# Optimization experiments

Hardware: AMD Instinct MI355X
Metric: run time of the kernel (lower is better)

Reference implementation:

```python
import jax, jax.numpy as jnp
import numpy as np

M, N = 4096, 4096  # placement density grid size (even, as the rfft-based kernel assumes)


def _expk(L):
    # precompute_expk(L): [cos(pi*k/(2L)), sin(pi*k/(2L))] stacked -> [L, 2]
    a = np.pi * np.arange(L) / (2.0 * L)
    return np.stack([np.cos(a), np.sin(a)], axis=-1).astype(np.float32)


def setup_inputs() -> dict:
    key = jax.random.key(0)
    x = jax.random.normal(key, (M, N), dtype=jnp.float32)
    return {
        "x": x,
        "expkM": jnp.asarray(_expk(M)),
        "expkN": jnp.asarray(_expk(N)),
    }


def _idct1d(x, expk):
    # Unnormalized IDCT (DCT-III with DC weight 1) along the last axis:
    #   y_u = sum_k x_k * cos(pi*k*(2u+1)/(2L))
    # Makhoul FFT trick: c_k = x_k * exp(i*pi*k/(2L)); v = L*ifft(c);
    #   y[2m] = Re(v[m]),  y[2m+1] = Re(v[L-1-m])
    L = x.shape[-1]
    ek = expk[:, 0] + 1j * expk[:, 1]            # exp(i*pi*k/(2L)), [L]
    v = (jnp.fft.ifft(x * ek, axis=-1) * L).real  # [..., L]
    half = L // 2
    even = v[..., :half]                          # y[0], y[2], ...
    odd = v[..., ::-1][..., :half]                # y[1], y[3], ... (= v[L-1], v[L-2], ...)
    return jnp.stack([even, odd], axis=-1).reshape(x.shape)


def reference(x, expkM, expkN):
    # out[u,v] = sum_{p,q} x[p,q] cos(pi*p*(2u+1)/(2M)) cos(pi*q*(2v+1)/(2N))
    t = _idct1d(x, expkN)                               # transform along N (last dim)
    out = _idct1d(t.swapaxes(-1, -2), expkM)            # transform along M
    return out.swapaxes(-1, -2)
```

## Files before the change

kernel.cpp:

```cpp
#include <hip/hip_runtime.h>
#include <stdint.h>

typedef __bf16 bf16x8_t __attribute__((ext_vector_type(8)));
typedef float f32x4_t __attribute__((ext_vector_type(4)));

__device__ __forceinline__ uint32_t f32_to_bf16_bits(float f) {
    union { float f; uint32_t u; } v; v.f = f;
    return (v.u + 0x7FFFu + ((v.u >> 16) & 1u)) >> 16;
}

__device__ __forceinline__ float bf16_bits_to_f32(uint32_t b) {
    union { uint32_t u; float f; } v; v.u = b << 16;
    return v.f;
}

__global__ void prep_kernel(const float* __restrict__ X,
                            unsigned short* __restrict__ Ae,
                            unsigned short* __restrict__ Ao,
                            unsigned short* __restrict__ Xe,
                            unsigned short* __restrict__ Xo) {
    if (blockIdx.x < 4096) {
        const int idx = blockIdx.x * 256 + threadIdx.x;
        const int sel = idx >> 19;
        const int e   = idx & ((1 << 19) - 1);
        const int n   = e >> 8;
        const int c0  = (e & 255) << 3;
        const uint32_t tn = (uint32_t)(2 * n + 1);
        unsigned short* dst = sel ? Ao : Ae;
        uint32_t packed[4];
#pragma unroll
        for (int jj = 0; jj < 4; ++jj) {
            uint32_t cA = (uint32_t)(c0 + 2 * jj);
            uint32_t cB = cA + 1;
            uint32_t r0 = ((2u * cA + (uint32_t)sel) * tn) & 16383u;
            uint32_t r1 = ((2u * cB + (uint32_t)sel) * tn) & 16383u;
            float v0 = __cosf((float)r0 * 3.8349519697141e-4f);
            float v1 = __cosf((float)r1 * 3.8349519697141e-4f);
            packed[jj] = f32_to_bf16_bits(v0) | (f32_to_bf16_bits(v1) << 16);
        }
        *(uint4*)(dst + (size_t)n * 2048 + c0) = make_uint4(packed[0], packed[1], packed[2], packed[3]);
    } else {
        const int idx = (blockIdx.x - 4096) * 256 + threadIdx.x;
        const int q   = idx >> 9;
        const int p0  = (idx & 511) << 3;
        const float4* src = (const float4*)(X + (size_t)q * 4096 + p0);
        float4 a = src[0];
        float4 b = src[1];
        uint2 ev, od;
        ev.x = f32_to_bf16_bits(a.x) | (f32_to_bf16_bits(a.z) << 16);
        ev.y = f32_to_bf16_bits(b.x) | (f32_to_bf16_bits(b.z) << 16);
        od.x = f32_to_bf16_bits(a.y) | (f32_to_bf16_bits(a.w) << 16);
        od.y = f32_to_bf16_bits(b.y) | (f32_to_bf16_bits(b.w) << 16);
        *(uint2*)(Xe + (size_t)q * 2048 + (p0 >> 1)) = ev;
        *(uint2*)(Xo + (size_t)q * 2048 + (p0 >> 1)) = od;
    }
}

#define GLL(gp, lp) __builtin_amdgcn_global_load_lds( \
        (const __attribute__((address_space(1))) uint32_t*)(gp), \
        (__attribute__((address_space(3))) uint32_t*)(lp), 16, 0, 0)

__global__ __launch_bounds__(512, 2)
void gemm256_kernel(const unsigned short* __restrict__ Ae,
                    const unsigned short* __restrict__ Ao,
                    const unsigned short* __restrict__ Be,
                    const unsigned short* __restrict__ Bo,
                    unsigned short* __restrict__ Ce,
                    unsigned short* __restrict__ Co) {
    constexpr int KD = 2048;
    __shared__ __attribute__((aligned(16))) unsigned short smem[2 * 32768];

    const int tid  = threadIdx.x;
    const int wave = tid >> 6;
    const int lane = tid & 63;
    const int wm   = wave >> 2;
    const int wn   = wave & 3;

    const int tile_m = blockIdx.y << 8;
    const int tile_c = blockIdx.x << 8;
    const int par    = blockIdx.z;

    const unsigned short* gA = (par ? Ao : Ae) + (size_t)tile_m * KD;
    const unsigned short* gB = (par ? Bo : Be) + (size_t)tile_c * KD;
    unsigned short*       gC = par ? Co : Ce;

    f32x4_t acc[8][4];
#pragma unroll
    for (int i = 0; i < 8; ++i)
#pragma unroll
        for (int j = 0; j < 4; ++j)
            acc[i][j] = (f32x4_t){0.f, 0.f, 0.f, 0.f};

    int src_off[4], lds_off[4];
#pragma unroll
    for (int k = 0; k < 4; ++k) {
        const int c   = tid + (k << 9);
        const int row = c >> 3;
        const int g   = (c & 7) ^ (row & 7);
        src_off[k] = row * KD + (g << 3);
        lds_off[k] = c << 3;
    }

    const int frow = lane & 15;
    const int sw   = frow & 7;
    const int gq   = lane >> 4;
    const int aRowB = (wm * 128 + frow) * 64;
    const int bRowB = (wn * 64  + frow) * 64;

#define STAGE_TILE(buf, kadv) do {                                            \
    _Pragma("unroll")                                                         \
    for (int k_ = 0; k_ < 4; ++k_)                                            \
        GLL(gA + (kadv) + src_off[k_], (buf) + lds_off[k_]);                  \
    _Pragma("unroll")                                                         \
    for (int k_ = 0; k_ < 4; ++k_)                                            \
        GLL(gB + (kadv) + src_off[k_], (buf) + 16384 + lds_off[k_]);          \
} while (0)

#define COMPUTE_TILE(buf) do {                                                \
    _Pragma("unroll")                                                         \
    for (int kh_ = 0; kh_ < 2; ++kh_) {                                       \
        const int so_ = (((kh_ << 2) + gq) ^ sw) << 3;                        \
        bf16x8_t af_[8], bf_[4];                                              \
        _Pragma("unroll")                                                     \
        for (int i_ = 0; i_ < 8; ++i_) af_[i_] = *(const bf16x8_t*)((buf) + aRowB + i_ * 1024 + so_); \
        _Pragma("unroll")                                                     \
        for (int j_ = 0; j_ < 4; ++j_) bf_[j_] = *(const bf16x8_t*)((buf) + 16384 + bRowB + j_ * 1024 + so_); \
        __builtin_amdgcn_s_setprio(1);                                        \
        _Pragma("unroll")                                                     \
        for (int i_ = 0; i_ < 8; ++i_)                                        \
            _Pragma("unroll")                                                 \
            for (int j_ = 0; j_ < 4; ++j_)                                    \
                acc[i_][j_] = __builtin_amdgcn_mfma_f32_16x16x32_bf16(af_[i_], bf_[j_], acc[i_][j_], 0, 0, 0); \
        __builtin_amdgcn_s_setprio(0);                                        \
    }                                                                         \
} while (0)

#define TILE_SYNC() do {                                                      \
    asm volatile("s_waitcnt vmcnt(0)" ::: "memory");                          \
    __builtin_amdgcn_s_barrier();                                             \
    asm volatile("" ::: "memory");                                            \
} while (0)

    STAGE_TILE(smem, 0);
    TILE_SYNC();

    int co = 0;
#pragma unroll 1
    for (int t = 0; t < 31; ++t) {
        STAGE_TILE(smem + (co ^ 32768), (size_t)(t + 1) << 6);
        COMPUTE_TILE(smem + co);
        TILE_SYNC();
        co ^= 32768;
    }
    COMPUTE_TILE(smem + co);

#undef STAGE_TILE
#undef COMPUTE_TILE
#undef TILE_SYNC

    const int orow = tile_m + wm * 128 + ((lane >> 4) << 2);
    const int ocol = tile_c + wn * 64 + (lane & 15);
#pragma unroll
    for (int i = 0; i < 8; ++i)
#pragma unroll
        for (int j = 0; j < 4; ++j)
#pragma unroll
            for (int r = 0; r < 4; ++r) {
                const int m = orow + i * 16 + r;
                const int w = ocol + j * 16;
                gC[(size_t)m * 4096 + w] = (unsigned short)f32_to_bf16_bits(acc[i][j][r]);
            }
}

__global__ void bfly1_kernel(const unsigned short* __restrict__ Ce,
                             const unsigned short* __restrict__ Co,
                             unsigned short* __restrict__ Te,
                             unsigned short* __restrict__ To) {
    const int m  = blockIdx.x;
    const int c0 = threadIdx.x << 4;
    const uint4 e0 = *(const uint4*)(Ce + (size_t)m * 4096 + c0);
    const uint4 e1 = *(const uint4*)(Ce + (size_t)m * 4096 + c0 + 8);
    const uint4 o0 = *(const uint4*)(Co + (size_t)m * 4096 + c0);
    const uint4 o1 = *(const uint4*)(Co + (size_t)m * 4096 + c0 + 8);
    const uint32_t eu[8] = {e0.x, e0.y, e0.z, e0.w, e1.x, e1.y, e1.z, e1.w};
    const uint32_t ou[8] = {o0.x, o0.y, o0.z, o0.w, o1.x, o1.y, o1.z, o1.w};
    uint32_t se[4], so_[4], de[4], do_[4];
#pragma unroll
    for (int u = 0; u < 4; ++u) {
        float eA = bf16_bits_to_f32(eu[2*u] & 0xFFFF),  oA = bf16_bits_to_f32(ou[2*u] & 0xFFFF);
        float eB = bf16_bits_to_f32(eu[2*u] >> 16),     oB = bf16_bits_to_f32(ou[2*u] >> 16);
        float eC = bf16_bits_to_f32(eu[2*u+1] & 0xFFFF),oC = bf16_bits_to_f32(ou[2*u+1] & 0xFFFF);
        float eD = bf16_bits_to_f32(eu[2*u+1] >> 16),   oD = bf16_bits_to_f32(ou[2*u+1] >> 16);
        se[u]  = f32_to_bf16_bits(eA + oA) | (f32_to_bf16_bits(eC + oC) << 16);
        so_[u] = f32_to_bf16_bits(eB + oB) | (f32_to_bf16_bits(eD + oD) << 16);
        de[u]  = f32_to_bf16_bits(eA - oA) | (f32_to_bf16_bits(eC - oC) << 16);
        do_[u] = f32_to_bf16_bits(eB - oB) | (f32_to_bf16_bits(eD - oD) << 16);
    }
    const size_t rs = (size_t)m * 2048 + (c0 >> 1);
    const size_t rd = (size_t)(4095 - m) * 2048 + (c0 >> 1);
    *(uint4*)(Te + rs) = make_uint4(se[0], se[1], se[2], se[3]);
    *(uint4*)(To + rs) = make_uint4(so_[0], so_[1], so_[2], so_[3]);
    *(uint4*)(Te + rd) = make_uint4(de[0], de[1], de[2], de[3]);
    *(uint4*)(To + rd) = make_uint4(do_[0], do_[1], do_[2], do_[3]);
}

__global__ void bfly2_kernel(const unsigned short* __restrict__ Ce,
                             const unsigned short* __restrict__ Co,
                             float* __restrict__ out) {
    const int m  = blockIdx.x;
    const int c0 = threadIdx.x << 4;
    const uint4 e0 = *(const uint4*)(Ce + (size_t)m * 4096 + c0);
    const uint4 e1 = *(const uint4*)(Ce + (size_t)m * 4096 + c0 + 8);
    const uint4 o0 = *(const uint4*)(Co + (size_t)m * 4096 + c0);
    const uint4 o1 = *(const uint4*)(Co + (size_t)m * 4096 + c0 + 8);
    const uint32_t eu[8] = {e0.x, e0.y, e0.z, e0.w, e1.x, e1.y, e1.z, e1.w};
    const uint32_t ou[8] = {o0.x, o0.y, o0.z, o0.w, o1.x, o1.y, o1.z, o1.w};
    float s[16], d[16];
#pragma unroll
    for (int u = 0; u < 8; ++u) {
        const float eL = bf16_bits_to_f32(eu[u] & 0xFFFF), oL = bf16_bits_to_f32(ou[u] & 0xFFFF);
        const float eH = bf16_bits_to_f32(eu[u] >> 16),    oH = bf16_bits_to_f32(ou[u] >> 16);
        s[2*u] = eL + oL; s[2*u+1] = eH + oH;
        d[2*u] = eL - oL; d[2*u+1] = eH - oH;
    }
    float* ps = out + (size_t)m * 4096 + c0;
    float* pd = out + (size_t)(4095 - m) * 4096 + c0;
#pragma unroll
    for (int u = 0; u < 4; ++u) {
        *(float4*)(ps + 4 * u) = make_float4(s[4*u], s[4*u+1], s[4*u+2], s[4*u+3]);
        *(float4*)(pd + 4 * u) = make_float4(d[4*u], d[4*u+1], d[4*u+2], d[4*u+3]);
    }
}

extern "C" void kernel_launch(void* const* d_in, const int* in_sizes, int n_in,
                              void* d_out, int out_size, void* d_ws, size_t ws_size,
                              hipStream_t stream) {
    const float* x = (const float*)d_in[0];
    char* ws = (char*)d_ws;
    const size_t MB = 1024 * 1024;
    unsigned short* Ae = (unsigned short*)(ws);
    unsigned short* Ao = (unsigned short*)(ws + 8 * MB);
    unsigned short* Xe = (unsigned short*)(ws + 16 * MB);
    unsigned short* Xo = (unsigned short*)(ws + 32 * MB);
    unsigned short* C1e = (unsigned short*)(ws + 48 * MB);
    unsigned short* C1o = (unsigned short*)(ws + 64 * MB);
    float* out = (float*)d_out;

    prep_kernel<<<12288, 256, 0, stream>>>(x, Ae, Ao, Xe, Xo);

    dim3 ggrid(16, 8, 2);
    gemm256_kernel<<<ggrid, 512, 0, stream>>>(Ae, Ao, Xe, Xo, C1e, C1o);
    bfly1_kernel<<<2048, 256, 0, stream>>>(C1e, C1o, Xe, Xo);
    gemm256_kernel<<<ggrid, 512, 0, stream>>>(Ae, Ao, Xe, Xo, C1e, C1o);
    bfly2_kernel<<<2048, 256, 0, stream>>>(C1e, C1o, out);
}
```

Baseline: 261.9 us.

## Split GEMM main loop into 8-phase ping-pong schedule with interleaved staging

```diff
diff --git a/kernel.cpp b/kernel.cpp
--- a/kernel.cpp
+++ b/kernel.cpp
@@ -107,56 +107,98 @@
     const int aRowB = (wm * 128 + frow) * 64;
     const int bRowB = (wn * 64  + frow) * 64;
 
-#define STAGE_TILE(buf, kadv) do {                                            \
-    _Pragma("unroll")                                                         \
-    for (int k_ = 0; k_ < 4; ++k_)                                            \
-        GLL(gA + (kadv) + src_off[k_], (buf) + lds_off[k_]);                  \
-    _Pragma("unroll")                                                         \
-    for (int k_ = 0; k_ < 4; ++k_)                                            \
-        GLL(gB + (kadv) + src_off[k_], (buf) + 16384 + lds_off[k_]);          \
+#define S_A0(b, kadv)  do { GLL(gA + (kadv) + src_off[0], (b) + lds_off[0]); \
+                            GLL(gA + (kadv) + src_off[2], (b) + lds_off[2]); } while (0)
+#define S_A1(b, kadv)  do { GLL(gA + (kadv) + src_off[1], (b) + lds_off[1]); \
+                            GLL(gA + (kadv) + src_off[3], (b) + lds_off[3]); } while (0)
+#define S_B01(b, kadv) do { GLL(gB + (kadv) + src_off[0], (b) + 16384 + lds_off[0]); \
+                            GLL(gB + (kadv) + src_off[1], (b) + 16384 + lds_off[1]); } while (0)
+#define S_B23(b, kadv) do { GLL(gB + (kadv) + src_off[2], (b) + 16384 + lds_off[2]); \
+                            GLL(gB + (kadv) + src_off[3], (b) + 16384 + lds_off[3]); } while (0)
+#define S_NONE ((void)0)
+
+    bf16x8_t bfr[4];
+
+#define PHASE(cb, mh, kh, LOADB, STAGE_STMT, VM) do {                          \
+    const int so_ = ((((kh) << 2) + gq) ^ sw) << 3;                            \
+    bf16x8_t af_[4];                                                           \
+    _Pragma("unroll")                                                          \
+    for (int i_ = 0; i_ < 4; ++i_)                                             \
+        af_[i_] = *(const bf16x8_t*)((cb) + aRowB + ((mh) * 4 + i_) * 1024 + so_); \
+    if (LOADB) {                                                               \
+        _Pragma("unroll")                                                      \
+        for (int j_ = 0; j_ < 4; ++j_)                                         \
+            bfr[j_] = *(const bf16x8_t*)((cb) + 16384 + bRowB + j_ * 1024 + so_); \
+    }                                                                          \
+    STAGE_STMT;                                                                \
+    asm volatile("" ::: "memory");                                             \
+    __builtin_amdgcn_s_barrier();                                              \
+    asm volatile("s_waitcnt lgkmcnt(0)" ::: "memory");                         \
+    __builtin_amdgcn_sched_barrier(0);                                         \
+    __builtin_amdgcn_s_setprio(1);                                             \
+    _Pragma("unroll")                                                          \
+    for (int i_ = 0; i_ < 4; ++i_)                                             \
+        _Pragma("unroll")                                                      \
+        for (int j_ = 0; j_ < 4; ++j_)                                         \
+            acc[(mh) * 4 + i_][j_] = __builtin_amdgcn_mfma_f32_16x16x32_bf16(  \
+                af_[i_], bfr[j_], acc[(mh) * 4 + i_][j_], 0, 0, 0);            \
+    __builtin_amdgcn_s_setprio(0);                                             \
+    if constexpr ((VM) == 4) asm volatile("s_waitcnt vmcnt(4)" ::: "memory");  \
+    else if constexpr ((VM) == 2) asm volatile("s_waitcnt vmcnt(2)" ::: "memory"); \
+    else if constexpr ((VM) == 0) asm volatile("s_waitcnt vmcnt(0)" ::: "memory"); \
+    asm volatile("" ::: "memory");                                             \
+    __builtin_amdgcn_s_barrier();                                              \
+    asm volatile("" ::: "memory");                                             \
 } while (0)
 
-#define COMPUTE_TILE(buf) do {                                                \
-    _Pragma("unroll")                                                         \
-    for (int kh_ = 0; kh_ < 2; ++kh_) {                                       \
-        const int so_ = (((kh_ << 2) + gq) ^ sw) << 3;                        \
-        bf16x8_t af_[8], bf_[4];                                              \
-        _Pragma("unroll")                                                     \
-        for (int i_ = 0; i_ < 8; ++i_) af_[i_] = *(const bf16x8_t*)((buf) + aRowB + i_ * 1024 + so_); \
-        _Pragma("unroll")                                                     \
-        for (int j_ = 0; j_ < 4; ++j_) bf_[j_] = *(const bf16x8_t*)((buf) + 16384 + bRowB + j_ * 1024 + so_); \
-        __builtin_amdgcn_s_setprio(1);                                        \
-        _Pragma("unroll")                                                     \
-        for (int i_ = 0; i_ < 8; ++i_)                                        \
-            _Pragma("unroll")                                                 \
-            for (int j_ = 0; j_ < 4; ++j_)                                    \
-                acc[i_][j_] = __builtin_amdgcn_mfma_f32_16x16x32_bf16(af_[i_], bf_[j_], acc[i_][j_], 0, 0, 0); \
-        __builtin_amdgcn_s_setprio(0);                                        \
-    }                                                                         \
+#define ITER_FULL(J) do {                                                      \
+    unsigned short* b0_ = smem;                                                \
+    unsigned short* b1_ = smem + 32768;                                        \
+    const int k1_ = (2 * (J) + 1) << 6;                                        \
+    const int k2_ = (2 * (J) + 2) << 6;                                        \
+    const int k3_ = (2 * (J) + 3) << 6;                                        \
+    PHASE(b0_, 0, 0, 1, S_B01(b1_, k1_), 4);                                   \
+    PHASE(b0_, 1, 0, 0, S_B23(b1_, k1_), -1);                                  \
+    PHASE(b0_, 0, 1, 1, S_A1 (b1_, k1_), -1);                                  \
+    PHASE(b0_, 1, 1, 0, S_A0 (b0_, k2_), 4);                                   \
+    PHASE(b1_, 0, 0, 1, S_B01(b0_, k2_), 4);                                   \
+    PHASE(b1_, 1, 0, 0, S_B23(b0_, k2_), -1);                                  \
+    PHASE(b1_, 0, 1, 1, S_A1 (b0_, k2_), -1);                                  \
+    PHASE(b1_, 1, 1, 0, S_A0 (b1_, k3_), 4);                                   \
 } while (0)
 
-#define TILE_SYNC() do {                                                      \
-    asm volatile("s_waitcnt vmcnt(0)" ::: "memory");                          \
-    __builtin_amdgcn_s_barrier();                                             \
-    asm volatile("" ::: "memory");                                            \
+#define ITER_TAIL() do {                                                       \
+    unsigned short* b0_ = smem;                                                \
+    unsigned short* b1_ = smem + 32768;                                        \
+    const int k1_ = 31 << 6;                                                   \
+    PHASE(b0_, 0, 0, 1, S_B01(b1_, k1_), 4);                                   \
+    PHASE(b0_, 1, 0, 0, S_B23(b1_, k1_), -1);                                  \
+    PHASE(b0_, 0, 1, 1, S_A1 (b1_, k1_), -1);                                  \
+    PHASE(b0_, 1, 1, 0, S_NONE, 2);                                            \
+    PHASE(b1_, 0, 0, 1, S_NONE, 0);                                            \
+    PHASE(b1_, 1, 0, 0, S_NONE, -1);                                           \
+    PHASE(b1_, 0, 1, 1, S_NONE, -1);                                           \
+    PHASE(b1_, 1, 1, 0, S_NONE, -1);                                           \
 } while (0)
 
-    STAGE_TILE(smem, 0);
-    TILE_SYNC();
-
-    int co = 0;
+    S_A0(smem, 0); S_A1(smem, 0); S_B01(smem, 0); S_B23(smem, 0);
+    S_A0(smem + 32768, 64);
+    asm volatile("s_waitcnt vmcnt(2)" ::: "memory");
+    __builtin_amdgcn_s_barrier();
+    asm volatile("" ::: "memory");
+
 #pragma unroll 1
-    for (int t = 0; t < 31; ++t) {
-        STAGE_TILE(smem + (co ^ 32768), (size_t)(t + 1) << 6);
-        COMPUTE_TILE(smem + co);
-        TILE_SYNC();
-        co ^= 32768;
-    }
-    COMPUTE_TILE(smem + co);
-
-#undef STAGE_TILE
-#undef COMPUTE_TILE
-#undef TILE_SYNC
+    for (int J = 0; J < 15; ++J) ITER_FULL(J);
+    ITER_TAIL();
+
+#undef ITER_TAIL
+#undef ITER_FULL
+#undef PHASE
+#undef S_NONE
+#undef S_B23
+#undef S_B01
+#undef S_A1
+#undef S_A0
 
     const int orow = tile_m + wm * 128 + ((lane >> 4) << 2);
     const int ocol = tile_c + wn * 64 + (lane & 15);
```

Result: no change. 263.2 us (+0.5%).

## Shrink GEMM tiles to 128x256 with BK=32 and remap blocks for XCD locality

Applied to the files above, without the earlier changes.

```diff
diff --git a/kernel.cpp b/kernel.cpp
--- a/kernel.cpp
+++ b/kernel.cpp
@@ -60,25 +60,27 @@
         (const __attribute__((address_space(1))) uint32_t*)(gp), \
         (__attribute__((address_space(3))) uint32_t*)(lp), 16, 0, 0)
 
-__global__ __launch_bounds__(512, 2)
-void gemm256_kernel(const unsigned short* __restrict__ Ae,
+__global__ __launch_bounds__(256, 2)
+void gemm128_kernel(const unsigned short* __restrict__ Ae,
                     const unsigned short* __restrict__ Ao,
                     const unsigned short* __restrict__ Be,
                     const unsigned short* __restrict__ Bo,
                     unsigned short* __restrict__ Ce,
                     unsigned short* __restrict__ Co) {
     constexpr int KD = 2048;
-    __shared__ __attribute__((aligned(16))) unsigned short smem[2 * 32768];
+    __shared__ __attribute__((aligned(16))) unsigned short smem[2 * 12288];
 
     const int tid  = threadIdx.x;
     const int wave = tid >> 6;
     const int lane = tid & 63;
-    const int wm   = wave >> 2;
-    const int wn   = wave & 3;
-
-    const int tile_m = blockIdx.y << 8;
-    const int tile_c = blockIdx.x << 8;
-    const int par    = blockIdx.z;
+
+    const int bid = blockIdx.x;
+    const int wg  = (bid & 7) * 64 + (bid >> 3);
+    const int par = wg >> 8;
+    const int ty  = (wg >> 4) & 15;
+    const int tx  = wg & 15;
+    const int tile_m = ty << 7;
+    const int tile_c = tx << 8;
 
     const unsigned short* gA = (par ? Ao : Ae) + (size_t)tile_m * KD;
     const unsigned short* gB = (par ? Bo : Be) + (size_t)tile_c * KD;
@@ -91,48 +93,53 @@
         for (int j = 0; j < 4; ++j)
             acc[i][j] = (f32x4_t){0.f, 0.f, 0.f, 0.f};
 
-    int src_off[4], lds_off[4];
+    int a_src[2], a_lds[2], b_src[4], b_lds[4];
+#pragma unroll
+    for (int k = 0; k < 2; ++k) {
+        const int c   = tid + (k << 8);
+        const int row = c >> 2;
+        const int g   = (c & 3) ^ (row & 3);
+        a_src[k] = row * KD + (g << 3);
+        a_lds[k] = c << 3;
+    }
 #pragma unroll
     for (int k = 0; k < 4; ++k) {
-        const int c   = tid + (k << 9);
-        const int row = c >> 3;
-        const int g   = (c & 7) ^ (row & 7);
-        src_off[k] = row * KD + (g << 3);
-        lds_off[k] = c << 3;
+        const int c   = tid + (k << 8);
+        const int row = c >> 2;
+        const int g   = (c & 3) ^ (row & 3);
+        b_src[k] = row * KD + (g << 3);
+        b_lds[k] = 4096 + (c << 3);
     }
 
     const int frow = lane & 15;
-    const int sw   = frow & 7;
+    const int sw3  = frow & 3;
     const int gq   = lane >> 4;
-    const int aRowB = (wm * 128 + frow) * 64;
-    const int bRowB = (wn * 64  + frow) * 64;
+    const int aRow = frow * 32;
+    const int bRow = 4096 + (wave * 64 + frow) * 32;
 
 #define STAGE_TILE(buf, kadv) do {                                            \
+    GLL(gA + (kadv) + a_src[0], (buf) + a_lds[0]);                            \
+    GLL(gA + (kadv) + a_src[1], (buf) + a_lds[1]);                            \
+    GLL(gB + (kadv) + b_src[0], (buf) + b_lds[0]);                            \
+    GLL(gB + (kadv) + b_src[1], (buf) + b_lds[1]);                            \
+    GLL(gB + (kadv) + b_src[2], (buf) + b_lds[2]);                            \
+    GLL(gB + (kadv) + b_src[3], (buf) + b_lds[3]);                            \
+} while (0)
+
+#define COMPUTE_TILE(buf) do {                                                \
+    const int so_ = (gq ^ sw3) << 3;                                          \
+    bf16x8_t af_[8], bf_[4];                                                  \
     _Pragma("unroll")                                                         \
-    for (int k_ = 0; k_ < 4; ++k_)                                            \
-        GLL(gA + (kadv) + src_off[k_], (buf) + lds_off[k_]);                  \
+    for (int i_ = 0; i_ < 8; ++i_) af_[i_] = *(const bf16x8_t*)((buf) + aRow + i_ * 512 + so_); \
     _Pragma("unroll")                                                         \
-    for (int k_ = 0; k_ < 4; ++k_)                                            \
-        GLL(gB + (kadv) + src_off[k_], (buf) + 16384 + lds_off[k_]);          \
-} while (0)
-
-#define COMPUTE_TILE(buf) do {                                                \
+    for (int j_ = 0; j_ < 4; ++j_) bf_[j_] = *(const bf16x8_t*)((buf) + bRow + j_ * 512 + so_); \
+    __builtin_amdgcn_s_setprio(1);                                            \
     _Pragma("unroll")                                                         \
-    for (int kh_ = 0; kh_ < 2; ++kh_) {                                       \
-        const int so_ = (((kh_ << 2) + gq) ^ sw) << 3;                        \
-        bf16x8_t af_[8], bf_[4];                                              \
+    for (int i_ = 0; i_ < 8; ++i_)                                            \
         _Pragma("unroll")                                                     \
-        for (int i_ = 0; i_ < 8; ++i_) af_[i_] = *(const bf16x8_t*)((buf) + aRowB + i_ * 1024 + so_); \
-        _Pragma("unroll")                                                     \
-        for (int j_ = 0; j_ < 4; ++j_) bf_[j_] = *(const bf16x8_t*)((buf) + 16384 + bRowB + j_ * 1024 + so_); \
-        __builtin_amdgcn_s_setprio(1);                                        \
-        _Pragma("unroll")                                                     \
-        for (int i_ = 0; i_ < 8; ++i_)                                        \
-            _Pragma("unroll")                                                 \
-            for (int j_ = 0; j_ < 4; ++j_)                                    \
-                acc[i_][j_] = __builtin_amdgcn_mfma_f32_16x16x32_bf16(af_[i_], bf_[j_], acc[i_][j_], 0, 0, 0); \
-        __builtin_amdgcn_s_setprio(0);                                        \
-    }                                                                         \
+        for (int j_ = 0; j_ < 4; ++j_)                                        \
+            acc[i_][j_] = __builtin_amdgcn_mfma_f32_16x16x32_bf16(af_[i_], bf_[j_], acc[i_][j_], 0, 0, 0); \
+    __builtin_amdgcn_s_setprio(0);                                            \
 } while (0)
 
 #define TILE_SYNC() do {                                                      \
@@ -146,11 +153,11 @@
 
     int co = 0;
 #pragma unroll 1
-    for (int t = 0; t < 31; ++t) {
-        STAGE_TILE(smem + (co ^ 32768), (size_t)(t + 1) << 6);
+    for (int t = 0; t < 63; ++t) {
+        STAGE_TILE(smem + (co ^ 12288), (t + 1) << 5);
         COMPUTE_TILE(smem + co);
         TILE_SYNC();
-        co ^= 32768;
+        co ^= 12288;
     }
     COMPUTE_TILE(smem + co);
 
@@ -158,8 +165,8 @@
 #undef COMPUTE_TILE
 #undef TILE_SYNC
 
-    const int orow = tile_m + wm * 128 + ((lane >> 4) << 2);
-    const int ocol = tile_c + wn * 64 + (lane & 15);
+    const int orow = tile_m + ((lane >> 4) << 2);
+    const int ocol = tile_c + wave * 64 + (lane & 15);
 #pragma unroll
     for (int i = 0; i < 8; ++i)
 #pragma unroll
@@ -248,9 +255,8 @@
 
     prep_kernel<<<12288, 256, 0, stream>>>(x, Ae, Ao, Xe, Xo);
 
-    dim3 ggrid(16, 8, 2);
-    gemm256_kernel<<<ggrid, 512, 0, stream>>>(Ae, Ao, Xe, Xo, C1e, C1o);
+    gemm128_kernel<<<512, 256, 0, stream>>>(Ae, Ao, Xe, Xo, C1e, C1o);
     bfly1_kernel<<<2048, 256, 0, stream>>>(C1e, C1o, Xe, Xo);
-    gemm256_kernel<<<ggrid, 512, 0, stream>>>(Ae, Ao, Xe, Xo, C1e, C1o);
+    gemm128_kernel<<<512, 256, 0, stream>>>(Ae, Ao, Xe, Xo, C1e, C1o);
     bfly2_kernel<<<2048, 256, 0, stream>>>(C1e, C1o, out);
 }
```

New measurement: 281.7 us. 7.6% more time.

## Restructure GEMM main loop into quadrant-interleaved schedule with in-place refill

Applied to the files above, without the earlier changes.

```diff
diff --git a/kernel.cpp b/kernel.cpp
--- a/kernel.cpp
+++ b/kernel.cpp
@@ -107,56 +107,96 @@
     const int aRowB = (wm * 128 + frow) * 64;
     const int bRowB = (wn * 64  + frow) * 64;
 
-#define STAGE_TILE(buf, kadv) do {                                            \
-    _Pragma("unroll")                                                         \
-    for (int k_ = 0; k_ < 4; ++k_)                                            \
-        GLL(gA + (kadv) + src_off[k_], (buf) + lds_off[k_]);                  \
-    _Pragma("unroll")                                                         \
-    for (int k_ = 0; k_ < 4; ++k_)                                            \
-        GLL(gB + (kadv) + src_off[k_], (buf) + 16384 + lds_off[k_]);          \
-} while (0)
-
-#define COMPUTE_TILE(buf) do {                                                \
-    _Pragma("unroll")                                                         \
-    for (int kh_ = 0; kh_ < 2; ++kh_) {                                       \
-        const int so_ = (((kh_ << 2) + gq) ^ sw) << 3;                        \
-        bf16x8_t af_[8], bf_[4];                                              \
-        _Pragma("unroll")                                                     \
-        for (int i_ = 0; i_ < 8; ++i_) af_[i_] = *(const bf16x8_t*)((buf) + aRowB + i_ * 1024 + so_); \
-        _Pragma("unroll")                                                     \
-        for (int j_ = 0; j_ < 4; ++j_) bf_[j_] = *(const bf16x8_t*)((buf) + 16384 + bRowB + j_ * 1024 + so_); \
-        __builtin_amdgcn_s_setprio(1);                                        \
-        _Pragma("unroll")                                                     \
-        for (int i_ = 0; i_ < 8; ++i_)                                        \
-            _Pragma("unroll")                                                 \
-            for (int j_ = 0; j_ < 4; ++j_)                                    \
-                acc[i_][j_] = __builtin_amdgcn_mfma_f32_16x16x32_bf16(af_[i_], bf_[j_], acc[i_][j_], 0, 0, 0); \
-        __builtin_amdgcn_s_setprio(0);                                        \
-    }                                                                         \
-} while (0)
-
-#define TILE_SYNC() do {                                                      \
-    asm volatile("s_waitcnt vmcnt(0)" ::: "memory");                          \
-    __builtin_amdgcn_s_barrier();                                             \
-    asm volatile("" ::: "memory");                                            \
-} while (0)
-
-    STAGE_TILE(smem, 0);
-    TILE_SYNC();
-
-    int co = 0;
+#define S_A0(b, kadv)  do { GLL(gA + (kadv) + src_off[0], (b) + lds_off[0]); \
+                            GLL(gA + (kadv) + src_off[2], (b) + lds_off[2]); } while (0)
+#define S_A1(b, kadv)  do { GLL(gA + (kadv) + src_off[1], (b) + lds_off[1]); \
+                            GLL(gA + (kadv) + src_off[3], (b) + lds_off[3]); } while (0)
+#define S_B01(b, kadv) do { GLL(gB + (kadv) + src_off[0], (b) + 16384 + lds_off[0]); \
+                            GLL(gB + (kadv) + src_off[1], (b) + 16384 + lds_off[1]); } while (0)
+#define S_B23(b, kadv) do { GLL(gB + (kadv) + src_off[2], (b) + 16384 + lds_off[2]); \
+                            GLL(gB + (kadv) + src_off[3], (b) + 16384 + lds_off[3]); } while (0)
+
+#define SLOT(kh) (((((kh) << 2) + gq) ^ sw) << 3)
+#define MEMF asm volatile("" ::: "memory")
+#define BAR  __builtin_amdgcn_s_barrier()
+
+    bf16x8_t am[8];
+    bf16x8_t bn0[4], bn1[4];
+
+#define RD_AM(cb, mh) do {                                                     \
+    _Pragma("unroll")                                                          \
+    for (int i_ = 0; i_ < 4; ++i_)                                             \
+        _Pragma("unroll")                                                      \
+        for (int kh_ = 0; kh_ < 2; ++kh_)                                      \
+            am[i_ * 2 + kh_] = *(const bf16x8_t*)((cb) + aRowB + ((mh) * 4 + i_) * 1024 + SLOT(kh_)); \
+} while (0)
+
+#define RD_B(cb, nh, dst) do {                                                 \
+    _Pragma("unroll")                                                          \
+    for (int j_ = 0; j_ < 2; ++j_)                                             \
+        _Pragma("unroll")                                                      \
+        for (int kh_ = 0; kh_ < 2; ++kh_)                                      \
+            dst[j_ * 2 + kh_] = *(const bf16x8_t*)((cb) + 16384 + bRowB + ((nh) * 2 + j_) * 1024 + SLOT(kh_)); \
+} while (0)
+
+#define MM(mh, nh, bsrc) do {                                                  \
+    __builtin_amdgcn_s_setprio(1);                                             \
+    _Pragma("unroll")                                                          \
+    for (int i_ = 0; i_ < 4; ++i_)                                             \
+        _Pragma("unroll")                                                      \
+        for (int j_ = 0; j_ < 2; ++j_)                                         \
+            _Pragma("unroll")                                                  \
+            for (int kh_ = 0; kh_ < 2; ++kh_)                                  \
+                acc[(mh) * 4 + i_][(nh) * 2 + j_] =                            \
+                    __builtin_amdgcn_mfma_f32_16x16x32_bf16(                   \
+                        am[i_ * 2 + kh_], bsrc[j_ * 2 + kh_],                  \
+                        acc[(mh) * 4 + i_][(nh) * 2 + j_], 0, 0, 0);           \
+    __builtin_amdgcn_s_setprio(0);                                             \
+} while (0)
+
+#define GROUP(cb, k2, STG, WN) do {                                            \
+    RD_AM(cb, 0); RD_B(cb, 0, bn0);                                            \
+    MEMF; BAR; MM(0, 0, bn0); MEMF; BAR;                                       \
+    RD_B(cb, 1, bn1);                                                          \
+    if (STG) S_A0(cb, k2);                                                     \
+    MEMF; BAR; MM(0, 1, bn1); MEMF; BAR;                                       \
+    RD_AM(cb, 1);                                                              \
+    if (STG) S_B01(cb, k2);                                                    \
+    MEMF; BAR; MM(1, 0, bn0); MEMF; BAR;                                       \
+    if (STG) { S_B23(cb, k2); S_A1(cb, k2); }                                  \
+    MEMF; BAR; MM(1, 1, bn1);                                                  \
+    if ((WN) == 8)      asm volatile("s_waitcnt vmcnt(8)" ::: "memory");       \
+    else if ((WN) == 0) asm volatile("s_waitcnt vmcnt(0)" ::: "memory");       \
+    MEMF; BAR;                                                                 \
+} while (0)
+
+    unsigned short* b0 = smem;
+    unsigned short* b1 = smem + 32768;
+
+    S_A0(b0, 0); S_B01(b0, 0); S_B23(b0, 0); S_A1(b0, 0);
+    S_A0(b1, 64); S_B01(b1, 64); S_B23(b1, 64); S_A1(b1, 64);
+    asm volatile("s_waitcnt vmcnt(8)" ::: "memory");
+    BAR; MEMF;
+
 #pragma unroll 1
-    for (int t = 0; t < 31; ++t) {
-        STAGE_TILE(smem + (co ^ 32768), (size_t)(t + 1) << 6);
-        COMPUTE_TILE(smem + co);
-        TILE_SYNC();
-        co ^= 32768;
-    }
-    COMPUTE_TILE(smem + co);
-
-#undef STAGE_TILE
-#undef COMPUTE_TILE
-#undef TILE_SYNC
+    for (int J = 0; J < 15; ++J) {
+        GROUP(b0, (2 * J + 2) << 6, 1, 8);
+        GROUP(b1, (2 * J + 3) << 6, 1, 8);
+    }
+    GROUP(b0, 0, 0, 0);
+    GROUP(b1, 0, 0, -1);
+
+#undef GROUP
+#undef MM
+#undef RD_B
+#undef RD_AM
+#undef BAR
+#undef MEMF
+#undef SLOT
+#undef S_B23
+#undef S_B01
+#undef S_A1
+#undef S_A0
 
     const int orow = tile_m + wm * 128 + ((lane >> 4) << 2);
     const int ocol = tile_c + wn * 64 + (lane & 15);
```

After: 264.0 us. No clear change (+0.8%).
